# Performance work log

Measured on AMD Instinct MI355X. Metric: run time of the kernel, lower is better.

Reference implementation:

```python
import jax, jax.numpy as jnp
import numpy as np

N = 100000   # nodes
E = 800000   # edges (avg degree ~8)
G = 64       # graphs in batch
F_IN = 64
H = 128
C = 4


def setup_inputs() -> dict:
    key = jax.random.key(0)
    ks = jax.random.split(key, 14)
    def w(k, fin, fout):
        return jax.random.normal(k, (fin, fout), dtype=jnp.float32) * (1.0 / np.sqrt(fin))
    inp = {
        "x": jax.random.normal(ks[0], (N, F_IN), dtype=jnp.float32),
        "W1": w(ks[1], F_IN, H), "b1": jnp.zeros((H,), jnp.float32),
        "W2": w(ks[2], H, H),    "b2": jnp.zeros((H,), jnp.float32),
        "W3": w(ks[3], H, H),    "b3": jnp.zeros((H,), jnp.float32),
        "fw1": w(ks[4], H, H),   "fb1": jnp.zeros((H,), jnp.float32),
        "fw2": w(ks[5], H, C),   "fb2": jnp.zeros((C,), jnp.float32),
        "edge_index": jax.random.randint(ks[6], (2, E), 0, N, dtype=jnp.int32),
        "batch": jnp.sort(jax.random.randint(ks[7], (N,), 0, G, dtype=jnp.int32)),
    }
    return inp


def gcn_conv(x, W, b, src, dst):
    """PyG GCNConv: linear transform, add self-loops, symmetric deg^-1/2 norm, scatter-add."""
    h = x @ W                                                    # [N, H]
    deg = jax.ops.segment_sum(jnp.ones((E,), x.dtype), dst, num_segments=N) + 1.0  # self-loop
    dinv = jax.lax.rsqrt(deg)                                    # [N]
    norm = dinv[src] * dinv[dst]                                 # [E]
    agg = jax.ops.segment_sum(h[src] * norm[:, None], dst, num_segments=N)
    agg = agg + h * (dinv * dinv)[:, None]                       # self-loop term (norm = 1/deg)
    return agg + b


def reference(x, W1, b1, W2, b2, W3, b3, fw1, fb1, fw2, fb2, edge_index, batch):
    src, dst = edge_index[0], edge_index[1]
    h = jax.nn.relu(gcn_conv(x, W1, b1, src, dst))
    h = jax.nn.relu(gcn_conv(h, W2, b2, src, dst))
    h = gcn_conv(h, W3, b3, src, dst)
    # global mean pool over graphs
    s = jax.ops.segment_sum(h, batch, num_segments=G)            # [G, H]
    cnt = jax.ops.segment_sum(jnp.ones((N,), h.dtype), batch, num_segments=G)
    pooled = s / jnp.maximum(cnt, 1.0)[:, None]
    z = jax.nn.relu(pooled @ fw1 + fb1)
    return z @ fw2 + fb2                                          # [G, C]
```

## Files before the change

### kernel.cpp

```cpp
#include <hip/hip_runtime.h>

#define N_NODES 100000
#define N_EDGES 800000
#define G_GRAPHS 64
#define F_INPUT 64
#define H_DIM 128
#define C_OUT 4
#define CSR_CAP 32
#define EDGE_BLOCKS (N_EDGES / 256)
#define CONV_BLOCKS ((N_NODES + 255) / 256)
#define WPACK_BLOCKS 20
#define FILL_SEG 8
#define FILL_CHUNKS 125
#define FILL_RANGE (N_NODES / FILL_SEG)
#define FILL_CHUNK (N_EDGES / FILL_CHUNKS)
#define FILL_BLOCKS (FILL_SEG * FILL_CHUNKS)
#define SEG_SPAN (FILL_RANGE * CSR_CAP)

typedef __attribute__((ext_vector_type(8))) short bf16x8;
typedef __attribute__((ext_vector_type(8))) unsigned short u16x8;
typedef __attribute__((ext_vector_type(4))) float f32x4;

__device__ inline unsigned short f2bf(float f) {
    union { float f; unsigned int u; } v; v.f = f;
    unsigned int u = v.u + 0x7FFFu + ((v.u >> 16) & 1u);
    return (unsigned short)(u >> 16);
}
__device__ inline float bf2f(unsigned short b) {
    union { unsigned int u; float f; } v; v.u = ((unsigned int)b) << 16;
    return v.f;
}
__device__ inline float2 unpack_pair(unsigned int u) {
    union { unsigned int u; float f; } a, b;
    a.u = u << 16; b.u = u & 0xFFFF0000u;
    float2 r; r.x = a.f; r.y = b.f; return r;
}
__device__ inline unsigned char f2fp8(float v) {
    int r = __builtin_amdgcn_cvt_pk_fp8_f32(v, 0.0f, 0, false);
    return (unsigned char)(r & 0xFF);
}

__device__ inline void wpack_one(const float* __restrict__ W, unsigned short* __restrict__ hi,
                                 unsigned short* __restrict__ lo, int K, int t)
{
    int lane = t & 63;
    int tile = t >> 6;
    int KS = K / 32;
    int ct = tile / KS, ks = tile % KS;
    int n  = ct * 16 + (lane & 15);
    int k0 = ks * 32 + (lane >> 4) * 8;
    #pragma unroll
    for (int j = 0; j < 8; j++) {
        float w = W[(k0 + j) * H_DIM + n];
        unsigned short h = f2bf(w);
        hi[t * 8 + j] = h;
        lo[t * 8 + j] = f2bf(w - bf2f(h));
    }
}

__global__ __launch_bounds__(256) void hist_kernel(
    const int* __restrict__ dst, int* __restrict__ cnt, int* __restrict__ paddr,
    const float* __restrict__ W1, const float* __restrict__ W2, const float* __restrict__ W3,
    unsigned short* __restrict__ w1hi, unsigned short* __restrict__ w1lo,
    unsigned short* __restrict__ w2hi, unsigned short* __restrict__ w2lo,
    unsigned short* __restrict__ w3hi, unsigned short* __restrict__ w3lo)
{
    int b = blockIdx.x;
    if (b < EDGE_BLOCKS) {
        int e = b * 256 + threadIdx.x;
        int d = dst[e];
        int sl = atomicAdd(&cnt[d], 1);
        paddr[e] = (sl < CSR_CAP) ? d * CSR_CAP + sl : -1;
        return;
    }
    b -= EDGE_BLOCKS;
    int t = b * 256 + threadIdx.x;
    if (t < 1024)       wpack_one(W1, w1hi, w1lo, F_INPUT, t);
    else if (t < 3072)  wpack_one(W2, w2hi, w2lo, H_DIM, t - 1024);
    else                wpack_one(W3, w3hi, w3lo, H_DIM, t - 3072);
}

__global__ __launch_bounds__(256) void prep_kernel(
    const int* __restrict__ paddr, const int* __restrict__ src,
    int* __restrict__ csr,
    const int* __restrict__ cnti, const float4* __restrict__ x4,
    float* __restrict__ dinv, unsigned int* __restrict__ xb_u,
    unsigned int* __restrict__ p1z, unsigned int* __restrict__ p3z)
{
    int b = blockIdx.x;
    if (b < FILL_BLOCKS) {
        const int r   = b & (FILL_SEG - 1);
        const int m   = b >> 3;
        const int plo = r * SEG_SPAN;
        const int phi = plo + SEG_SPAN;
        const int e0  = m * FILL_CHUNK;
        for (int e = e0 + threadIdx.x; e < e0 + FILL_CHUNK; e += 256) {
            int pa = paddr[e];
            if (pa >= plo && pa < phi)
                csr[pa] = src[e];
        }
        return;
    }
    b -= FILL_BLOCKS;
    __shared__ float dl[256];
    int i = b * 256 + threadIdx.x;
    float dv = 0.0f;
    if (i < N_NODES) {
        int c  = cnti[i];
        int dc = min(c, CSR_CAP);
        dv = rsqrtf((float)c + 1.0f);
        dinv[i] = dv;
        int pad = (dc + 7) & ~7;
        for (int s2 = dc; s2 < pad; s2++)
            csr[(size_t)i * CSR_CAP + s2] = N_NODES;
    } else if (i == N_NODES) {
        for (int c = 0; c < 32; c++) {
            xb_u[(size_t)N_NODES * 32 + c] = 0u;
            p1z [(size_t)N_NODES * 32 + c] = 0u;
            p3z [(size_t)N_NODES * 32 + c] = 0u;
        }
    }
    dl[threadIdx.x] = dv;
    __syncthreads();
    const int row_base = b * 256;
    for (int c = threadIdx.x; c < 256 * 16; c += 256) {
        int r = c >> 4;
        int row = row_base + r;
        if (row < N_NODES) {
            float d2 = dl[r];
            float4 v = x4[(size_t)row * 16 + (c & 15)];
            size_t o = ((size_t)row * 16 + (c & 15)) * 2;
            xb_u[o + 0] = (unsigned int)f2bf(v.x * d2) | ((unsigned int)f2bf(v.y * d2) << 16);
            xb_u[o + 1] = (unsigned int)f2bf(v.z * d2) | ((unsigned int)f2bf(v.w * d2) << 16);
        }
    }
}

__global__ __launch_bounds__(256) void gather1_kernel(
    const unsigned int* __restrict__ xb_u, const int* __restrict__ cnti,
    const int* __restrict__ csr, const float* __restrict__ dinv,
    unsigned int* __restrict__ outb)
{
    int idx = blockIdx.x * 256 + threadIdx.x;
    int i  = idx >> 5;
    int f2 = idx & 31;
    int dc = min(cnti[i], CSR_CAP);
    int beg  = i * CSR_CAP;
    int end8 = beg + ((dc + 7) & ~7);
    float2 acc = unpack_pair(xb_u[(size_t)i * 32 + f2]);
    for (int e = beg; e < end8; e += 8) {
        int4 c0 = *(const int4*)(csr + e);
        int4 c1 = *(const int4*)(csr + e + 4);
        float2 v0 = unpack_pair(xb_u[(size_t)c0.x * 32 + f2]);
        float2 v1 = unpack_pair(xb_u[(size_t)c0.y * 32 + f2]);
        float2 v2 = unpack_pair(xb_u[(size_t)c0.z * 32 + f2]);
        float2 v3 = unpack_pair(xb_u[(size_t)c0.w * 32 + f2]);
        float2 v4 = unpack_pair(xb_u[(size_t)c1.x * 32 + f2]);
        float2 v5 = unpack_pair(xb_u[(size_t)c1.y * 32 + f2]);
        float2 v6 = unpack_pair(xb_u[(size_t)c1.z * 32 + f2]);
        float2 v7 = unpack_pair(xb_u[(size_t)c1.w * 32 + f2]);
        acc.x += ((v0.x + v1.x) + (v2.x + v3.x)) + ((v4.x + v5.x) + (v6.x + v7.x));
        acc.y += ((v0.y + v1.y) + (v2.y + v3.y)) + ((v4.y + v5.y) + (v6.y + v7.y));
    }
    float dv = dinv[i];
    outb[idx] = (unsigned int)f2bf(acc.x * dv) | ((unsigned int)f2bf(acc.y * dv) << 16);
}

__device__ inline void acc_u2(uint2 w, float* __restrict__ a) {
    auto l0 = __builtin_amdgcn_cvt_pk_f32_fp8(w.x, false);
    auto h0 = __builtin_amdgcn_cvt_pk_f32_fp8(w.x, true);
    auto l1 = __builtin_amdgcn_cvt_pk_f32_fp8(w.y, false);
    auto h1 = __builtin_amdgcn_cvt_pk_f32_fp8(w.y, true);
    a[0] += l0[0]; a[1] += l0[1]; a[2] += h0[0]; a[3] += h0[1];
    a[4] += l1[0]; a[5] += l1[1]; a[6] += h1[0]; a[7] += h1[1];
}
__device__ inline void gather_fp8_u2(
    const uint2* __restrict__ base, const int* __restrict__ csr,
    int i, int beg, int end8, float* __restrict__ a)
{
    acc_u2(base[(size_t)i * 16], a);
    for (int e = beg; e < end8; e += 8) {
        int4 c0 = *(const int4*)(csr + e);
        int4 c1 = *(const int4*)(csr + e + 4);
        uint2 w0 = base[(size_t)c0.x * 16];
        uint2 w1 = base[(size_t)c0.y * 16];
        uint2 w2 = base[(size_t)c0.z * 16];
        uint2 w3 = base[(size_t)c0.w * 16];
        uint2 w4 = base[(size_t)c1.x * 16];
        uint2 w5 = base[(size_t)c1.y * 16];
        uint2 w6 = base[(size_t)c1.z * 16];
        uint2 w7 = base[(size_t)c1.w * 16];
        acc_u2(w0, a); acc_u2(w1, a); acc_u2(w2, a); acc_u2(w3, a);
        acc_u2(w4, a); acc_u2(w5, a); acc_u2(w6, a); acc_u2(w7, a);
    }
}

__global__ __launch_bounds__(256) void gather2_kernel(
    const uint2* __restrict__ hs8, const int* __restrict__ cnti,
    const int* __restrict__ csr, const float* __restrict__ dinv,
    const float* __restrict__ bias, uint2* __restrict__ out8)
{
    int idx = blockIdx.x * 256 + threadIdx.x;
    int i  = idx >> 4;
    int f8 = idx & 15;
    int dc = min(cnti[i], CSR_CAP);
    int beg  = i * CSR_CAP;
    int end8 = beg + ((dc + 7) & ~7);
    float a[8] = {0, 0, 0, 0, 0, 0, 0, 0};
    gather_fp8_u2(hs8 + f8, csr, i, beg, end8, a);
    float dv = dinv[i];
    float4 b0 = *(const float4*)(bias + f8 * 8);
    float4 b1 = *(const float4*)(bias + f8 * 8 + 4);
    float v0 = fmaxf(a[0] * dv + b0.x, 0.0f);
    float v1 = fmaxf(a[1] * dv + b0.y, 0.0f);
    float v2 = fmaxf(a[2] * dv + b0.z, 0.0f);
    float v3 = fmaxf(a[3] * dv + b0.w, 0.0f);
    float v4 = fmaxf(a[4] * dv + b1.x, 0.0f);
    float v5 = fmaxf(a[5] * dv + b1.y, 0.0f);
    float v6 = fmaxf(a[6] * dv + b1.z, 0.0f);
    float v7 = fmaxf(a[7] * dv + b1.w, 0.0f);
    int d0 = __builtin_amdgcn_cvt_pk_fp8_f32(v0, v1, 0, false);
    d0 = __builtin_amdgcn_cvt_pk_fp8_f32(v2, v3, d0, true);
    int d1 = __builtin_amdgcn_cvt_pk_fp8_f32(v4, v5, 0, false);
    d1 = __builtin_amdgcn_cvt_pk_fp8_f32(v6, v7, d1, true);
    uint2 o; o.x = (unsigned int)d0; o.y = (unsigned int)d1;
    out8[(size_t)i * 16 + f8] = o;
}

__global__ __launch_bounds__(256) void gather3_kernel(
    const uint2* __restrict__ hs8, const int* __restrict__ cnti,
    const int* __restrict__ csr, const float* __restrict__ dinv,
    const float* __restrict__ bias, uint4* __restrict__ outb)
{
    int idx = blockIdx.x * 256 + threadIdx.x;
    int i  = idx >> 4;
    int f8 = idx & 15;
    int dc = min(cnti[i], CSR_CAP);
    int beg  = i * CSR_CAP;
    int end8 = beg + ((dc + 7) & ~7);
    float a[8] = {0, 0, 0, 0, 0, 0, 0, 0};
    gather_fp8_u2(hs8 + f8, csr, i, beg, end8, a);
    float dv = dinv[i];
    float4 b0 = *(const float4*)(bias + f8 * 8);
    float4 b1 = *(const float4*)(bias + f8 * 8 + 4);
    uint4 o;
    o.x = (unsigned int)f2bf(a[0] * dv + b0.x) | ((unsigned int)f2bf(a[1] * dv + b0.y) << 16);
    o.y = (unsigned int)f2bf(a[2] * dv + b0.z) | ((unsigned int)f2bf(a[3] * dv + b0.w) << 16);
    o.z = (unsigned int)f2bf(a[4] * dv + b1.x) | ((unsigned int)f2bf(a[5] * dv + b1.y) << 16);
    o.w = (unsigned int)f2bf(a[6] * dv + b1.z) | ((unsigned int)f2bf(a[7] * dv + b1.w) << 16);
    outb[(size_t)i * 16 + f8] = o;
}

template <int K, bool BIAS_RELU, bool IN_FP8>
__global__ __launch_bounds__(256) void mfma_gemm_kernel(
    const void* __restrict__ inv, const unsigned short* __restrict__ whi,
    const unsigned short* __restrict__ wlo, const float* __restrict__ dinv,
    const float* __restrict__ bias, unsigned char* __restrict__ out8)
{
    constexpr int KS = K / 32;
    __shared__ unsigned short As[128 * K];

    const int tid  = threadIdx.x;
    const int row0 = blockIdx.x * 128;

    const int CH = 128 * K / 8;
    for (int c = tid; c < CH; c += 256) {
        int mt   = c / (KS * 64);
        int rest = c % (KS * 64);
        int ks   = rest / 64;
        int ln   = rest % 64;
        int r    = mt * 16 + (ln & 15);
        int k    = ks * 32 + (ln >> 4) * 8;
        int gr   = row0 + r; if (gr >= N_NODES) gr = N_NODES - 1;
        if constexpr (IN_FP8) {
            const unsigned char* in8 = (const unsigned char*)inv;
            uint2 t = *(const uint2*)(in8 + (size_t)gr * K + k);
            auto f0 = __builtin_amdgcn_cvt_pk_f32_fp8(t.x, false);
            auto f1 = __builtin_amdgcn_cvt_pk_f32_fp8(t.x, true);
            auto f2 = __builtin_amdgcn_cvt_pk_f32_fp8(t.y, false);
            auto f3 = __builtin_amdgcn_cvt_pk_f32_fp8(t.y, true);
            unsigned int* Au = (unsigned int*)(As + c * 8);
            Au[0] = (unsigned int)f2bf(f0[0]) | ((unsigned int)f2bf(f0[1]) << 16);
            Au[1] = (unsigned int)f2bf(f1[0]) | ((unsigned int)f2bf(f1[1]) << 16);
            Au[2] = (unsigned int)f2bf(f2[0]) | ((unsigned int)f2bf(f2[1]) << 16);
            Au[3] = (unsigned int)f2bf(f3[0]) | ((unsigned int)f2bf(f3[1]) << 16);
        } else {
            const unsigned short* in16 = (const unsigned short*)inv;
            *(u16x8*)(As + c * 8) = *(const u16x8*)(in16 + (size_t)gr * K + k);
        }
    }
    __syncthreads();

    const int w = tid >> 6, lane = tid & 63;
    const int quad = lane >> 4, l16 = lane & 15;

    f32x4 acc[2][8];
    #pragma unroll
    for (int rt = 0; rt < 2; rt++)
        #pragma unroll
        for (int ct = 0; ct < 8; ct++) acc[rt][ct] = (f32x4)(0.0f);

    #pragma unroll
    for (int ks = 0; ks < KS; ks++) {
        bf16x8 a0 = *(const bf16x8*)(As + (((w * 2 + 0) * KS + ks) * 64 + lane) * 8);
        bf16x8 a1 = *(const bf16x8*)(As + (((w * 2 + 1) * KS + ks) * 64 + lane) * 8);
        bf16x8 bh[8], bl[8];
        #pragma unroll
        for (int ct = 0; ct < 8; ct++) {
            bh[ct] = *(const bf16x8*)(whi + ((size_t)(ct * KS + ks) * 64 + lane) * 8);
            bl[ct] = *(const bf16x8*)(wlo + ((size_t)(ct * KS + ks) * 64 + lane) * 8);
        }
        #pragma unroll
        for (int ct = 0; ct < 8; ct++) {
            acc[0][ct] = __builtin_amdgcn_mfma_f32_16x16x32_bf16(a0, bh[ct], acc[0][ct], 0, 0, 0);
            acc[0][ct] = __builtin_amdgcn_mfma_f32_16x16x32_bf16(a0, bl[ct], acc[0][ct], 0, 0, 0);
            acc[1][ct] = __builtin_amdgcn_mfma_f32_16x16x32_bf16(a1, bh[ct], acc[1][ct], 0, 0, 0);
            acc[1][ct] = __builtin_amdgcn_mfma_f32_16x16x32_bf16(a1, bl[ct], acc[1][ct], 0, 0, 0);
        }
    }

    float bv[8];
    if (BIAS_RELU) {
        #pragma unroll
        for (int ct = 0; ct < 8; ct++) bv[ct] = bias[ct * 16 + l16];
    }

    #pragma unroll
    for (int rt = 0; rt < 2; rt++) {
        #pragma unroll
        for (int reg = 0; reg < 4; reg++) {
            int row = row0 + w * 32 + rt * 16 + quad * 4 + reg;
            if (row < N_NODES) {
                float dv = BIAS_RELU ? 0.0f : dinv[row];
                #pragma unroll
                for (int ct = 0; ct < 8; ct++) {
                    float val;
                    if (BIAS_RELU) val = fmaxf(acc[rt][ct][reg] + bv[ct], 0.0f);
                    else           val = acc[rt][ct][reg] * dv;
                    out8[(size_t)row * H_DIM + ct * 16 + l16] = f2fp8(val);
                }
            }
        }
    }
}

__global__ __launch_bounds__(128) void pool_kernel(
    const unsigned short* __restrict__ A, const int* __restrict__ batch,
    float* __restrict__ s, float* __restrict__ cnt)
{
    const int RPB = 32;
    int row0 = blockIdx.x * RPB;
    int f = threadIdx.x;
    int g0 = batch[row0];
    int g1 = batch[row0 + RPB - 1];
    if (g0 == g1) {
        float acc = 0.0f;
        #pragma unroll
        for (int r = 0; r < RPB; r++)
            acc += bf2f(A[(size_t)(row0 + r) * H_DIM + f]);
        unsafeAtomicAdd(&s[g0 * H_DIM + f], acc);
        if (f == 0) unsafeAtomicAdd(&cnt[g0], (float)RPB);
    } else {
        float acc = 0.0f;
        int cur = g0, c = 0;
        for (int r = 0; r < RPB; r++) {
            int g = batch[row0 + r];
            if (g != cur) {
                unsafeAtomicAdd(&s[cur * H_DIM + f], acc);
                if (f == 0) unsafeAtomicAdd(&cnt[cur], (float)c);
                cur = g; acc = 0.0f; c = 0;
            }
            acc += bf2f(A[(size_t)(row0 + r) * H_DIM + f]);
            c++;
        }
        unsafeAtomicAdd(&s[cur * H_DIM + f], acc);
        if (f == 0) unsafeAtomicAdd(&cnt[cur], (float)c);
    }
}

__global__ __launch_bounds__(128) void mlp_kernel(
    const float* __restrict__ s, const float* __restrict__ cnt,
    const float* __restrict__ fw1, const float* __restrict__ fb1,
    const float* __restrict__ fw2, const float* __restrict__ fb2,
    float* __restrict__ out)
{
    __shared__ float p[H_DIM];
    __shared__ float z[H_DIM];
    int g = blockIdx.x;
    int f = threadIdx.x;
    float c = fmaxf(cnt[g], 1.0f);
    p[f] = s[g * H_DIM + f] / c;
    __syncthreads();
    float acc = fb1[f];
    for (int k = 0; k < H_DIM; k++) acc = fmaf(p[k], fw1[k * H_DIM + f], acc);
    z[f] = fmaxf(acc, 0.0f);
    __syncthreads();
    if (f < C_OUT) {
        float o = fb2[f];
        for (int k = 0; k < H_DIM; k++) o = fmaf(z[k], fw2[k * C_OUT + f], o);
        out[g * C_OUT + f] = o;
    }
}

extern "C" void kernel_launch(void* const* d_in, const int* in_sizes, int n_in,
                              void* d_out, int out_size, void* d_ws, size_t ws_size,
                              hipStream_t stream)
{
    const float* x   = (const float*)d_in[0];
    const float* W1  = (const float*)d_in[1];
    const float* b1  = (const float*)d_in[2];
    const float* W2  = (const float*)d_in[3];
    const float* b2  = (const float*)d_in[4];
    const float* W3  = (const float*)d_in[5];
    const float* b3  = (const float*)d_in[6];
    const float* fw1 = (const float*)d_in[7];
    const float* fb1 = (const float*)d_in[8];
    const float* fw2 = (const float*)d_in[9];
    const float* fb2 = (const float*)d_in[10];
    const int*   ei  = (const int*)d_in[11];
    const int*   bat = (const int*)d_in[12];
    const int* esrc = ei;
    const int* edst = ei + N_EDGES;
    float* out = (float*)d_out;

    char* ws = (char*)d_ws;
    unsigned short* xb   = (unsigned short*)ws; ws += (size_t)(N_NODES + 1) * F_INPUT * 2;
    unsigned short* aggA = (unsigned short*)ws; ws += (size_t)N_NODES * F_INPUT * 2;
    unsigned short* aggB = (unsigned short*)ws; ws += (size_t)N_NODES * H_DIM * 2;
    unsigned char*  p0 = (unsigned char*)ws;  ws += (size_t)(N_NODES + 1) * H_DIM;
    unsigned char*  p1 = (unsigned char*)ws;  ws += (size_t)(N_NODES + 1) * H_DIM;
    unsigned char*  p2 = (unsigned char*)ws;  ws += (size_t)(N_NODES + 1) * H_DIM;
    unsigned char*  p3 = (unsigned char*)ws;  ws += (size_t)(N_NODES + 1) * H_DIM;
    unsigned short* w1hi = (unsigned short*)ws; ws += H_DIM * F_INPUT * 2;
    unsigned short* w1lo = (unsigned short*)ws; ws += H_DIM * F_INPUT * 2;
    unsigned short* w2hi = (unsigned short*)ws; ws += H_DIM * H_DIM * 2;
    unsigned short* w2lo = (unsigned short*)ws; ws += H_DIM * H_DIM * 2;
    unsigned short* w3hi = (unsigned short*)ws; ws += H_DIM * H_DIM * 2;
    unsigned short* w3lo = (unsigned short*)ws; ws += H_DIM * H_DIM * 2;
    float* dinv = (float*)ws;  ws += N_NODES * 4;
    int* paddr  = (int*)ws;    ws += (size_t)N_EDGES * 4;
    int* csr    = (int*)ws;    ws += (size_t)N_NODES * CSR_CAP * 4;
    int*   cnti = (int*)ws;    ws += N_NODES * 4;
    float* s    = (float*)ws;  ws += G_GRAPHS * H_DIM * 4;
    float* cnt  = (float*)ws;  ws += G_GRAPHS * 4;

    hipMemsetAsync(cnti, 0, (N_NODES + G_GRAPHS * H_DIM + G_GRAPHS) * sizeof(int), stream);

    hist_kernel<<<EDGE_BLOCKS + WPACK_BLOCKS, 256, 0, stream>>>(
        edst, cnti, paddr, W1, W2, W3, w1hi, w1lo, w2hi, w2lo, w3hi, w3lo);
    prep_kernel<<<FILL_BLOCKS + CONV_BLOCKS, 256, 0, stream>>>(
        paddr, esrc, csr, cnti, (const float4*)x, dinv, (unsigned int*)xb,
        (unsigned int*)p1, (unsigned int*)p3);

    const int gemm_grid = (N_NODES + 127) / 128;

    gather1_kernel<<<(N_NODES * 32) / 256, 256, 0, stream>>>(
        (const unsigned int*)xb, cnti, csr, dinv, (unsigned int*)aggA);
    mfma_gemm_kernel<64, true, false><<<gemm_grid, 256, 0, stream>>>(
        aggA, w1hi, w1lo, dinv, b1, p0);
    mfma_gemm_kernel<128, false, true><<<gemm_grid, 256, 0, stream>>>(
        p0, w2hi, w2lo, dinv, nullptr, p1);
    gather2_kernel<<<(N_NODES * 16) / 256, 256, 0, stream>>>(
        (const uint2*)p1, cnti, csr, dinv, b2, (uint2*)p2);
    mfma_gemm_kernel<128, false, true><<<gemm_grid, 256, 0, stream>>>(
        p2, w3hi, w3lo, dinv, nullptr, p3);
    gather3_kernel<<<(N_NODES * 16) / 256, 256, 0, stream>>>(
        (const uint2*)p3, cnti, csr, dinv, b3, (uint4*)aggB);

    pool_kernel<<<N_NODES / 32, 128, 0, stream>>>(aggB, bat, s, cnt);
    mlp_kernel<<<G_GRAPHS, 128, 0, stream>>>(s, cnt, fw1, fb1, fw2, fb2, out);
}
```

Before: 309.5 us.

## Fuse neighbor gather into following MFMA GEMM for layers one and three

Replaces the separate gather1+GEMM1 and gather2+GEMM3 kernel pairs with fused kernels. Each 1024-thread block gathers 128 node rows from CSR into shared memory in MFMA-ready bf16 layout, then runs the split-hi/lo bf16 MFMA GEMM directly. This removes two intermediate global round trips (aggA and p2) and two launches. In exchange, gather threads now load 16-byte vectors per neighbor, and the large blocks may lower occupancy while GEMM waves wait on the gather phase.

Measured after the change: 346.2 us. 11.8% more time.

```diff
diff --git a/kernel.cpp b/kernel.cpp
--- a/kernel.cpp
+++ b/kernel.cpp
@@ -136,34 +136,216 @@
     }
 }
 
-__global__ __launch_bounds__(256) void gather1_kernel(
-    const unsigned int* __restrict__ xb_u, const int* __restrict__ cnti,
-    const int* __restrict__ csr, const float* __restrict__ dinv,
-    unsigned int* __restrict__ outb)
-{
-    int idx = blockIdx.x * 256 + threadIdx.x;
-    int i  = idx >> 5;
-    int f2 = idx & 31;
-    int dc = min(cnti[i], CSR_CAP);
-    int beg  = i * CSR_CAP;
-    int end8 = beg + ((dc + 7) & ~7);
-    float2 acc = unpack_pair(xb_u[(size_t)i * 32 + f2]);
+__device__ inline void acc_bf8(uint4 w, float* __restrict__ a) {
+    float2 p0 = unpack_pair(w.x), p1 = unpack_pair(w.y);
+    float2 p2 = unpack_pair(w.z), p3 = unpack_pair(w.w);
+    a[0] += p0.x; a[1] += p0.y; a[2] += p1.x; a[3] += p1.y;
+    a[4] += p2.x; a[5] += p2.y; a[6] += p3.x; a[7] += p3.y;
+}
+__device__ inline void acc16(uint4 w, float* __restrict__ a) {
+    auto l0 = __builtin_amdgcn_cvt_pk_f32_fp8(w.x, false);
+    auto h0 = __builtin_amdgcn_cvt_pk_f32_fp8(w.x, true);
+    auto l1 = __builtin_amdgcn_cvt_pk_f32_fp8(w.y, false);
+    auto h1 = __builtin_amdgcn_cvt_pk_f32_fp8(w.y, true);
+    auto l2 = __builtin_amdgcn_cvt_pk_f32_fp8(w.z, false);
+    auto h2 = __builtin_amdgcn_cvt_pk_f32_fp8(w.z, true);
+    auto l3 = __builtin_amdgcn_cvt_pk_f32_fp8(w.w, false);
+    auto h3 = __builtin_amdgcn_cvt_pk_f32_fp8(w.w, true);
+    a[0]  += l0[0]; a[1]  += l0[1]; a[2]  += h0[0]; a[3]  += h0[1];
+    a[4]  += l1[0]; a[5]  += l1[1]; a[6]  += h1[0]; a[7]  += h1[1];
+    a[8]  += l2[0]; a[9]  += l2[1]; a[10] += h2[0]; a[11] += h2[1];
+    a[12] += l3[0]; a[13] += l3[1]; a[14] += h3[0]; a[15] += h3[1];
+}
+__device__ inline void gather_fp8_u4(
+    const uint4* __restrict__ base, const int* __restrict__ csr,
+    int i, int beg, int end8, float* __restrict__ a)
+{
+    acc16(base[(size_t)i * 8], a);
     for (int e = beg; e < end8; e += 8) {
         int4 c0 = *(const int4*)(csr + e);
         int4 c1 = *(const int4*)(csr + e + 4);
-        float2 v0 = unpack_pair(xb_u[(size_t)c0.x * 32 + f2]);
-        float2 v1 = unpack_pair(xb_u[(size_t)c0.y * 32 + f2]);
-        float2 v2 = unpack_pair(xb_u[(size_t)c0.z * 32 + f2]);
-        float2 v3 = unpack_pair(xb_u[(size_t)c0.w * 32 + f2]);
-        float2 v4 = unpack_pair(xb_u[(size_t)c1.x * 32 + f2]);
-        float2 v5 = unpack_pair(xb_u[(size_t)c1.y * 32 + f2]);
-        float2 v6 = unpack_pair(xb_u[(size_t)c1.z * 32 + f2]);
-        float2 v7 = unpack_pair(xb_u[(size_t)c1.w * 32 + f2]);
-        acc.x += ((v0.x + v1.x) + (v2.x + v3.x)) + ((v4.x + v5.x) + (v6.x + v7.x));
-        acc.y += ((v0.y + v1.y) + (v2.y + v3.y)) + ((v4.y + v5.y) + (v6.y + v7.y));
-    }
-    float dv = dinv[i];
-    outb[idx] = (unsigned int)f2bf(acc.x * dv) | ((unsigned int)f2bf(acc.y * dv) << 16);
+        uint4 w0 = base[(size_t)c0.x * 8];
+        uint4 w1 = base[(size_t)c0.y * 8];
+        uint4 w2 = base[(size_t)c0.z * 8];
+        uint4 w3 = base[(size_t)c0.w * 8];
+        uint4 w4 = base[(size_t)c1.x * 8];
+        uint4 w5 = base[(size_t)c1.y * 8];
+        uint4 w6 = base[(size_t)c1.z * 8];
+        uint4 w7 = base[(size_t)c1.w * 8];
+        acc16(w0, a); acc16(w1, a); acc16(w2, a); acc16(w3, a);
+        acc16(w4, a); acc16(w5, a); acc16(w6, a); acc16(w7, a);
+    }
+}
+
+__global__ __launch_bounds__(1024) void gemm_g1_kernel(
+    const uint4* __restrict__ xb4, const int* __restrict__ cnti,
+    const int* __restrict__ csr, const float* __restrict__ dinv,
+    const unsigned short* __restrict__ whi, const unsigned short* __restrict__ wlo,
+    const float* __restrict__ bias, unsigned char* __restrict__ out8)
+{
+    constexpr int KS = 2;
+    __shared__ unsigned short As[128 * 64];
+    uint4* As4 = (uint4*)As;
+    const int tid  = threadIdx.x;
+    const int row0 = blockIdx.x * 128;
+
+    {
+        int r = tid >> 3, f16 = tid & 7;
+        int gr = row0 + r; if (gr >= N_NODES) gr = N_NODES - 1;
+        int dc = min(cnti[gr], CSR_CAP);
+        int beg  = gr * CSR_CAP;
+        int end8 = beg + ((dc + 7) & ~7);
+        const uint4* base = xb4 + f16;
+        float a[8];
+        {
+            uint4 w = base[(size_t)gr * 8];
+            float2 p0 = unpack_pair(w.x), p1 = unpack_pair(w.y);
+            float2 p2 = unpack_pair(w.z), p3 = unpack_pair(w.w);
+            a[0] = p0.x; a[1] = p0.y; a[2] = p1.x; a[3] = p1.y;
+            a[4] = p2.x; a[5] = p2.y; a[6] = p3.x; a[7] = p3.y;
+        }
+        for (int e = beg; e < end8; e += 8) {
+            int4 c0 = *(const int4*)(csr + e);
+            int4 c1 = *(const int4*)(csr + e + 4);
+            uint4 w0 = base[(size_t)c0.x * 8];
+            uint4 w1 = base[(size_t)c0.y * 8];
+            uint4 w2 = base[(size_t)c0.z * 8];
+            uint4 w3 = base[(size_t)c0.w * 8];
+            uint4 w4 = base[(size_t)c1.x * 8];
+            uint4 w5 = base[(size_t)c1.y * 8];
+            uint4 w6 = base[(size_t)c1.z * 8];
+            uint4 w7 = base[(size_t)c1.w * 8];
+            acc_bf8(w0, a); acc_bf8(w1, a); acc_bf8(w2, a); acc_bf8(w3, a);
+            acc_bf8(w4, a); acc_bf8(w5, a); acc_bf8(w6, a); acc_bf8(w7, a);
+        }
+        float dv = dinv[gr];
+        uint4 o;
+        o.x = (unsigned int)f2bf(a[0] * dv) | ((unsigned int)f2bf(a[1] * dv) << 16);
+        o.y = (unsigned int)f2bf(a[2] * dv) | ((unsigned int)f2bf(a[3] * dv) << 16);
+        o.z = (unsigned int)f2bf(a[4] * dv) | ((unsigned int)f2bf(a[5] * dv) << 16);
+        o.w = (unsigned int)f2bf(a[6] * dv) | ((unsigned int)f2bf(a[7] * dv) << 16);
+        int mt = r >> 4, l16r = r & 15;
+        As4[(mt * KS + (f16 >> 2)) * 64 + (f16 & 3) * 16 + l16r] = o;
+    }
+    __syncthreads();
+
+    const int w = tid >> 6, lane = tid & 63;
+    const int quad = lane >> 4, l16 = lane & 15;
+    const int mt = w >> 1, ct0 = (w & 1) * 4;
+
+    f32x4 acc[4];
+    #pragma unroll
+    for (int c = 0; c < 4; c++) acc[c] = (f32x4)(0.0f);
+    #pragma unroll
+    for (int ks = 0; ks < KS; ks++) {
+        bf16x8 a0 = *(const bf16x8*)(As + ((mt * KS + ks) * 64 + lane) * 8);
+        bf16x8 bh[4], bl[4];
+        #pragma unroll
+        for (int c = 0; c < 4; c++) {
+            bh[c] = *(const bf16x8*)(whi + ((size_t)((ct0 + c) * KS + ks) * 64 + lane) * 8);
+            bl[c] = *(const bf16x8*)(wlo + ((size_t)((ct0 + c) * KS + ks) * 64 + lane) * 8);
+        }
+        #pragma unroll
+        for (int c = 0; c < 4; c++) {
+            acc[c] = __builtin_amdgcn_mfma_f32_16x16x32_bf16(a0, bh[c], acc[c], 0, 0, 0);
+            acc[c] = __builtin_amdgcn_mfma_f32_16x16x32_bf16(a0, bl[c], acc[c], 0, 0, 0);
+        }
+    }
+    float bv[4];
+    #pragma unroll
+    for (int c = 0; c < 4; c++) bv[c] = bias[(ct0 + c) * 16 + l16];
+    #pragma unroll
+    for (int reg = 0; reg < 4; reg++) {
+        int row = row0 + mt * 16 + quad * 4 + reg;
+        if (row < N_NODES) {
+            #pragma unroll
+            for (int c = 0; c < 4; c++) {
+                float val = fmaxf(acc[c][reg] + bv[c], 0.0f);
+                out8[(size_t)row * H_DIM + (ct0 + c) * 16 + l16] = f2fp8(val);
+            }
+        }
+    }
+}
+
+__global__ __launch_bounds__(1024) void gemm_g2_kernel(
+    const uint4* __restrict__ hs8, const int* __restrict__ cnti,
+    const int* __restrict__ csr, const float* __restrict__ dinv,
+    const unsigned short* __restrict__ whi, const unsigned short* __restrict__ wlo,
+    const float* __restrict__ bias, unsigned char* __restrict__ out8)
+{
+    constexpr int KS = 4;
+    __shared__ unsigned short As[128 * 128];
+    uint4* As4 = (uint4*)As;
+    const int tid  = threadIdx.x;
+    const int row0 = blockIdx.x * 128;
+
+    {
+        int r = tid >> 3, f16 = tid & 7;
+        int gr = row0 + r; if (gr >= N_NODES) gr = N_NODES - 1;
+        int dc = min(cnti[gr], CSR_CAP);
+        int beg  = gr * CSR_CAP;
+        int end8 = beg + ((dc + 7) & ~7);
+        float a[16] = {0,0,0,0,0,0,0,0,0,0,0,0,0,0,0,0};
+        gather_fp8_u4(hs8 + f16, csr, gr, beg, end8, a);
+        float dv = dinv[gr];
+        const float4* bb = (const float4*)(bias + f16 * 16);
+        float4 b0 = bb[0], b1 = bb[1], b2 = bb[2], b3 = bb[3];
+        float v0  = fmaxf(a[0]  * dv + b0.x, 0.0f), v1  = fmaxf(a[1]  * dv + b0.y, 0.0f);
+        float v2  = fmaxf(a[2]  * dv + b0.z, 0.0f), v3  = fmaxf(a[3]  * dv + b0.w, 0.0f);
+        float v4  = fmaxf(a[4]  * dv + b1.x, 0.0f), v5  = fmaxf(a[5]  * dv + b1.y, 0.0f);
+        float v6  = fmaxf(a[6]  * dv + b1.z, 0.0f), v7  = fmaxf(a[7]  * dv + b1.w, 0.0f);
+        float v8  = fmaxf(a[8]  * dv + b2.x, 0.0f), v9  = fmaxf(a[9]  * dv + b2.y, 0.0f);
+        float v10 = fmaxf(a[10] * dv + b2.z, 0.0f), v11 = fmaxf(a[11] * dv + b2.w, 0.0f);
+        float v12 = fmaxf(a[12] * dv + b3.x, 0.0f), v13 = fmaxf(a[13] * dv + b3.y, 0.0f);
+        float v14 = fmaxf(a[14] * dv + b3.z, 0.0f), v15 = fmaxf(a[15] * dv + b3.w, 0.0f);
+        uint4 o0, o1;
+        o0.x = (unsigned int)f2bf(v0)  | ((unsigned int)f2bf(v1)  << 16);
+        o0.y = (unsigned int)f2bf(v2)  | ((unsigned int)f2bf(v3)  << 16);
+        o0.z = (unsigned int)f2bf(v4)  | ((unsigned int)f2bf(v5)  << 16);
+        o0.w = (unsigned int)f2bf(v6)  | ((unsigned int)f2bf(v7)  << 16);
+        o1.x = (unsigned int)f2bf(v8)  | ((unsigned int)f2bf(v9)  << 16);
+        o1.y = (unsigned int)f2bf(v10) | ((unsigned int)f2bf(v11) << 16);
+        o1.z = (unsigned int)f2bf(v12) | ((unsigned int)f2bf(v13) << 16);
+        o1.w = (unsigned int)f2bf(v14) | ((unsigned int)f2bf(v15) << 16);
+        int mt = r >> 4, l16r = r & 15;
+        int bi = (mt * KS + (f16 >> 1)) * 64 + ((f16 & 1) * 2) * 16 + l16r;
+        As4[bi]      = o0;
+        As4[bi + 16] = o1;
+    }
+    __syncthreads();
+
+    const int w = tid >> 6, lane = tid & 63;
+    const int quad = lane >> 4, l16 = lane & 15;
+    const int mt = w >> 1, ct0 = (w & 1) * 4;
+
+    f32x4 acc[4];
+    #pragma unroll
+    for (int c = 0; c < 4; c++) acc[c] = (f32x4)(0.0f);
+    #pragma unroll
+    for (int ks = 0; ks < KS; ks++) {
+        bf16x8 a0 = *(const bf16x8*)(As + ((mt * KS + ks) * 64 + lane) * 8);
+        bf16x8 bh[4], bl[4];
+        #pragma unroll
+        for (int c = 0; c < 4; c++) {
+            bh[c] = *(const bf16x8*)(whi + ((size_t)((ct0 + c) * KS + ks) * 64 + lane) * 8);
+            bl[c] = *(const bf16x8*)(wlo + ((size_t)((ct0 + c) * KS + ks) * 64 + lane) * 8);
+        }
+        #pragma unroll
+        for (int c = 0; c < 4; c++) {
+            acc[c] = __builtin_amdgcn_mfma_f32_16x16x32_bf16(a0, bh[c], acc[c], 0, 0, 0);
+            acc[c] = __builtin_amdgcn_mfma_f32_16x16x32_bf16(a0, bl[c], acc[c], 0, 0, 0);
+        }
+    }
+    #pragma unroll
+    for (int reg = 0; reg < 4; reg++) {
+        int row = row0 + mt * 16 + quad * 4 + reg;
+        if (row < N_NODES) {
+            float dvr = dinv[row];
+            #pragma unroll
+            for (int c = 0; c < 4; c++)
+                out8[(size_t)row * H_DIM + (ct0 + c) * 16 + l16] = f2fp8(acc[c][reg] * dvr);
+        }
+    }
 }
 
 __device__ inline void acc_u2(uint2 w, float* __restrict__ a) {
@@ -193,38 +375,6 @@
         acc_u2(w0, a); acc_u2(w1, a); acc_u2(w2, a); acc_u2(w3, a);
         acc_u2(w4, a); acc_u2(w5, a); acc_u2(w6, a); acc_u2(w7, a);
     }
-}
-
-__global__ __launch_bounds__(256) void gather2_kernel(
-    const uint2* __restrict__ hs8, const int* __restrict__ cnti,
-    const int* __restrict__ csr, const float* __restrict__ dinv,
-    const float* __restrict__ bias, uint2* __restrict__ out8)
-{
-    int idx = blockIdx.x * 256 + threadIdx.x;
-    int i  = idx >> 4;
-    int f8 = idx & 15;
-    int dc = min(cnti[i], CSR_CAP);
-    int beg  = i * CSR_CAP;
-    int end8 = beg + ((dc + 7) & ~7);
-    float a[8] = {0, 0, 0, 0, 0, 0, 0, 0};
-    gather_fp8_u2(hs8 + f8, csr, i, beg, end8, a);
-    float dv = dinv[i];
-    float4 b0 = *(const float4*)(bias + f8 * 8);
-    float4 b1 = *(const float4*)(bias + f8 * 8 + 4);
-    float v0 = fmaxf(a[0] * dv + b0.x, 0.0f);
-    float v1 = fmaxf(a[1] * dv + b0.y, 0.0f);
-    float v2 = fmaxf(a[2] * dv + b0.z, 0.0f);
-    float v3 = fmaxf(a[3] * dv + b0.w, 0.0f);
-    float v4 = fmaxf(a[4] * dv + b1.x, 0.0f);
-    float v5 = fmaxf(a[5] * dv + b1.y, 0.0f);
-    float v6 = fmaxf(a[6] * dv + b1.z, 0.0f);
-    float v7 = fmaxf(a[7] * dv + b1.w, 0.0f);
-    int d0 = __builtin_amdgcn_cvt_pk_fp8_f32(v0, v1, 0, false);
-    d0 = __builtin_amdgcn_cvt_pk_fp8_f32(v2, v3, d0, true);
-    int d1 = __builtin_amdgcn_cvt_pk_fp8_f32(v4, v5, 0, false);
-    d1 = __builtin_amdgcn_cvt_pk_fp8_f32(v6, v7, d1, true);
-    uint2 o; o.x = (unsigned int)d0; o.y = (unsigned int)d1;
-    out8[(size_t)i * 16 + f8] = o;
 }
 
 __global__ __launch_bounds__(256) void gather3_kernel(
@@ -425,11 +575,9 @@
 
     char* ws = (char*)d_ws;
     unsigned short* xb   = (unsigned short*)ws; ws += (size_t)(N_NODES + 1) * F_INPUT * 2;
-    unsigned short* aggA = (unsigned short*)ws; ws += (size_t)N_NODES * F_INPUT * 2;
     unsigned short* aggB = (unsigned short*)ws; ws += (size_t)N_NODES * H_DIM * 2;
     unsigned char*  p0 = (unsigned char*)ws;  ws += (size_t)(N_NODES + 1) * H_DIM;
     unsigned char*  p1 = (unsigned char*)ws;  ws += (size_t)(N_NODES + 1) * H_DIM;
-    unsigned char*  p2 = (unsigned char*)ws;  ws += (size_t)(N_NODES + 1) * H_DIM;
     unsigned char*  p3 = (unsigned char*)ws;  ws += (size_t)(N_NODES + 1) * H_DIM;
     unsigned short* w1hi = (unsigned short*)ws; ws += H_DIM * F_INPUT * 2;
     unsigned short* w1lo = (unsigned short*)ws; ws += H_DIM * F_INPUT * 2;
@@ -454,16 +602,12 @@
 
     const int gemm_grid = (N_NODES + 127) / 128;
 
-    gather1_kernel<<<(N_NODES * 32) / 256, 256, 0, stream>>>(
-        (const unsigned int*)xb, cnti, csr, dinv, (unsigned int*)aggA);
-    mfma_gemm_kernel<64, true, false><<<gemm_grid, 256, 0, stream>>>(
-        aggA, w1hi, w1lo, dinv, b1, p0);
+    gemm_g1_kernel<<<gemm_grid, 1024, 0, stream>>>(
+        (const uint4*)xb, cnti, csr, dinv, w1hi, w1lo, b1, p0);
     mfma_gemm_kernel<128, false, true><<<gemm_grid, 256, 0, stream>>>(
         p0, w2hi, w2lo, dinv, nullptr, p1);
-    gather2_kernel<<<(N_NODES * 16) / 256, 256, 0, stream>>>(
-        (const uint2*)p1, cnti, csr, dinv, b2, (uint2*)p2);
-    mfma_gemm_kernel<128, false, true><<<gemm_grid, 256, 0, stream>>>(
-        p2, w3hi, w3lo, dinv, nullptr, p3);
+    gemm_g2_kernel<<<gemm_grid, 1024, 0, stream>>>(
+        (const uint4*)p1, cnti, csr, dinv, w3hi, w3lo, b2, p3);
     gather3_kernel<<<(N_NODES * 16) / 256, 256, 0, stream>>>(
         (const uint2*)p3, cnti, csr, dinv, b3, (uint4*)aggB);
 
```

## Fuse mean-pool into MLP kernel via binary search over sorted batch

Applied to the files above, without the earlier changes.

Replaces the atomic-based pool kernel and separate MLP kernel with one kernel per graph that locates its node range by binary search on the sorted batch vector and sums rows directly. This removes the atomics, the s/cnt workspace and part of the memset, and saves one launch. It also retunes the CSR fill partition to fewer segments and more edge chunks. The cost is that pooling now runs on only 64 blocks, each serially reading roughly 1.5k rows, which greatly reduces parallelism for that stage.

New measurement: 359.5 us. +16.1%, slower.

```diff
diff --git a/kernel.cpp b/kernel.cpp
--- a/kernel.cpp
+++ b/kernel.cpp
@@ -10,8 +10,8 @@
 #define EDGE_BLOCKS (N_EDGES / 256)
 #define CONV_BLOCKS ((N_NODES + 255) / 256)
 #define WPACK_BLOCKS 20
-#define FILL_SEG 8
-#define FILL_CHUNKS 125
+#define FILL_SEG 4
+#define FILL_CHUNKS 250
 #define FILL_RANGE (N_NODES / FILL_SEG)
 #define FILL_CHUNK (N_EDGES / FILL_CHUNKS)
 #define FILL_BLOCKS (FILL_SEG * FILL_CHUNKS)
@@ -90,7 +90,7 @@
     int b = blockIdx.x;
     if (b < FILL_BLOCKS) {
         const int r   = b & (FILL_SEG - 1);
-        const int m   = b >> 3;
+        const int m   = b >> 2;
         const int plo = r * SEG_SPAN;
         const int phi = plo + SEG_SPAN;
         const int e0  = m * FILL_CHUNK;
@@ -344,56 +344,46 @@
     }
 }
 
-__global__ __launch_bounds__(128) void pool_kernel(
-    const unsigned short* __restrict__ A, const int* __restrict__ batch,
-    float* __restrict__ s, float* __restrict__ cnt)
-{
-    const int RPB = 32;
-    int row0 = blockIdx.x * RPB;
-    int f = threadIdx.x;
-    int g0 = batch[row0];
-    int g1 = batch[row0 + RPB - 1];
-    if (g0 == g1) {
-        float acc = 0.0f;
-        #pragma unroll
-        for (int r = 0; r < RPB; r++)
-            acc += bf2f(A[(size_t)(row0 + r) * H_DIM + f]);
-        unsafeAtomicAdd(&s[g0 * H_DIM + f], acc);
-        if (f == 0) unsafeAtomicAdd(&cnt[g0], (float)RPB);
-    } else {
-        float acc = 0.0f;
-        int cur = g0, c = 0;
-        for (int r = 0; r < RPB; r++) {
-            int g = batch[row0 + r];
-            if (g != cur) {
-                unsafeAtomicAdd(&s[cur * H_DIM + f], acc);
-                if (f == 0) unsafeAtomicAdd(&cnt[cur], (float)c);
-                cur = g; acc = 0.0f; c = 0;
-            }
-            acc += bf2f(A[(size_t)(row0 + r) * H_DIM + f]);
-            c++;
-        }
-        unsafeAtomicAdd(&s[cur * H_DIM + f], acc);
-        if (f == 0) unsafeAtomicAdd(&cnt[cur], (float)c);
-    }
-}
-
-__global__ __launch_bounds__(128) void mlp_kernel(
-    const float* __restrict__ s, const float* __restrict__ cnt,
+__global__ __launch_bounds__(128) void poolmlp_kernel(
+    const unsigned short* __restrict__ A, const int* __restrict__ bat,
     const float* __restrict__ fw1, const float* __restrict__ fb1,
     const float* __restrict__ fw2, const float* __restrict__ fb2,
     float* __restrict__ out)
 {
     __shared__ float p[H_DIM];
     __shared__ float z[H_DIM];
-    int g = blockIdx.x;
-    int f = threadIdx.x;
-    float c = fmaxf(cnt[g], 1.0f);
-    p[f] = s[g * H_DIM + f] / c;
+    const int g = blockIdx.x;
+    const int f = threadIdx.x;
+
+    int l = 0, r = N_NODES;
+    while (l < r) { int m = (l + r) >> 1; if (bat[m] < g) l = m + 1; else r = m; }
+    const int lo = l;
+    r = N_NODES;
+    while (l < r) { int m = (l + r) >> 1; if (bat[m] < g + 1) l = m + 1; else r = m; }
+    const int hi = l;
+
+    float acc = 0.0f;
+    int row = lo;
+    for (; row + 8 <= hi; row += 8) {
+        float a0 = bf2f(A[(size_t)(row + 0) * H_DIM + f]);
+        float a1 = bf2f(A[(size_t)(row + 1) * H_DIM + f]);
+        float a2 = bf2f(A[(size_t)(row + 2) * H_DIM + f]);
+        float a3 = bf2f(A[(size_t)(row + 3) * H_DIM + f]);
+        float a4 = bf2f(A[(size_t)(row + 4) * H_DIM + f]);
+        float a5 = bf2f(A[(size_t)(row + 5) * H_DIM + f]);
+        float a6 = bf2f(A[(size_t)(row + 6) * H_DIM + f]);
+        float a7 = bf2f(A[(size_t)(row + 7) * H_DIM + f]);
+        acc += ((a0 + a1) + (a2 + a3)) + ((a4 + a5) + (a6 + a7));
+    }
+    for (; row < hi; row++)
+        acc += bf2f(A[(size_t)row * H_DIM + f]);
+
+    float c = fmaxf((float)(hi - lo), 1.0f);
+    p[f] = acc / c;
     __syncthreads();
-    float acc = fb1[f];
-    for (int k = 0; k < H_DIM; k++) acc = fmaf(p[k], fw1[k * H_DIM + f], acc);
-    z[f] = fmaxf(acc, 0.0f);
+    float acc1 = fb1[f];
+    for (int k = 0; k < H_DIM; k++) acc1 = fmaf(p[k], fw1[k * H_DIM + f], acc1);
+    z[f] = fmaxf(acc1, 0.0f);
     __syncthreads();
     if (f < C_OUT) {
         float o = fb2[f];
@@ -441,10 +431,8 @@
     int* paddr  = (int*)ws;    ws += (size_t)N_EDGES * 4;
     int* csr    = (int*)ws;    ws += (size_t)N_NODES * CSR_CAP * 4;
     int*   cnti = (int*)ws;    ws += N_NODES * 4;
-    float* s    = (float*)ws;  ws += G_GRAPHS * H_DIM * 4;
-    float* cnt  = (float*)ws;  ws += G_GRAPHS * 4;
-
-    hipMemsetAsync(cnti, 0, (N_NODES + G_GRAPHS * H_DIM + G_GRAPHS) * sizeof(int), stream);
+
+    hipMemsetAsync(cnti, 0, N_NODES * sizeof(int), stream);
 
     hist_kernel<<<EDGE_BLOCKS + WPACK_BLOCKS, 256, 0, stream>>>(
         edst, cnti, paddr, W1, W2, W3, w1hi, w1lo, w2hi, w2lo, w3hi, w3lo);
@@ -467,6 +455,6 @@
     gather3_kernel<<<(N_NODES * 16) / 256, 256, 0, stream>>>(
         (const uint2*)p3, cnti, csr, dinv, b3, (uint4*)aggB);
 
-    pool_kernel<<<N_NODES / 32, 128, 0, stream>>>(aggB, bat, s, cnt);
-    mlp_kernel<<<G_GRAPHS, 128, 0, stream>>>(s, cnt, fw1, fb1, fw2, fb2, out);
-}
+    poolmlp_kernel<<<G_GRAPHS, 128, 0, stream>>>(
+        aggB, bat, fw1, fb1, fw2, fb2, out);
+}
```
